# Optimization experiments

Measured on AMD Instinct MI355X. Metric: run time of the kernel, lower is better.

## Reference

```python
import jax, jax.numpy as jnp
import numpy as np

B, N, T, D, H = 32, 64, 16, 256, 256  # batch, actors, frames, feat dim, hidden_dim


def setup_inputs() -> dict:
    key = jax.random.key(0)
    ks = jax.random.split(key, 6)
    s = lambda fan: 1.0 / np.sqrt(fan)
    return {
        "x": jax.random.normal(ks[0], (B, N, T, D), jnp.float32),
        "W1_t": jax.random.normal(ks[1], (T * D, H), jnp.float32) * s(T * D),
        "b1_t": jnp.zeros((H,), jnp.float32),
        "W2_t": jax.random.normal(ks[2], (H, H), jnp.float32) * s(H),
        "b2_t": jnp.zeros((H,), jnp.float32),
        "W1_i": jax.random.normal(ks[3], (2 * H, H), jnp.float32) * s(2 * H),
        "b1_i": jnp.zeros((H,), jnp.float32),
        "W2_i": jax.random.normal(ks[4], (H, H), jnp.float32) * s(H),
        "b2_i": jnp.zeros((H,), jnp.float32),
    }


def reference(x, W1_t, b1_t, W2_t, b2_t, W1_i, b1_i, W2_i, b2_i):
    b, n, t, d = x.shape
    # STTR_trans output is immediately detached in the original; modeled as
    # identity + stop_gradient (view(N,B,T,-1) then view-back is a no-op on data).
    pf = jax.lax.stop_gradient(x)  # [B, N, T, D]

    # time_track_projection: MLP(T*D -> H -> H), ReLU between layers, no BN, eval dropout.
    h = jax.nn.relu(pf.reshape(b * n, t * d) @ W1_t + b1_t)
    person_feature = (h @ W2_t + b2_t).reshape(b, n, -1)  # [B, N, H]

    # relation_indexes: row-major enumeration of ordered pairs (i, j), j != i.
    # tem1 row N*i+j holds feature i, tem2 row N*i+j holds feature j.
    ii, jj = np.nonzero(~np.eye(n, dtype=bool))  # each [N*(N-1)], row-major order
    pair = jnp.concatenate(
        [person_feature[:, ii, :], person_feature[:, jj, :]], axis=-1
    )  # [B, N*(N-1), 2H] -- gather avoids materializing the full N*N grid

    # interaction_track_projection: MLP(2H -> H -> H)
    hi = jax.nn.relu(pair @ W1_i + b1_i)
    relation_feature = hi @ W2_i + b2_i  # [B, N*(N-1), H]

    return relation_feature, pf, person_feature
```

## Files before the change

### kernel.cpp

```cpp
#include <hip/hip_runtime.h>
#include <stdint.h>

typedef unsigned short u16;
typedef __attribute__((ext_vector_type(4))) float f32x4;
typedef __attribute__((ext_vector_type(8))) short bf16x8;
typedef __attribute__((ext_vector_type(4))) unsigned short u16x4;

#define DEV static __device__ __forceinline__

DEV u16 f2bf(float f) {
  union { float f; uint32_t u; } v; v.f = f;
  uint32_t u = v.u;
  return (u16)((u + 0x7FFFu + ((u >> 16) & 1u)) >> 16);
}

__global__ __launch_bounds__(256) void k_fuse_cast(const float* __restrict__ x,
                                                   float* __restrict__ pf,
                                                   u16* __restrict__ xb) {
  int i = blockIdx.x * 256 + threadIdx.x;
  f32x4 v = *(const f32x4*)(x + i * 4);
  *(f32x4*)(pf + i * 4) = v;
  u16x4 o;
  #pragma unroll
  for (int e = 0; e < 4; ++e) o[e] = f2bf(v[e]);
  *(u16x4*)(xb + i * 4) = o;
}

__global__ __launch_bounds__(256) void k_prep(const float* __restrict__ W1t,
                                              const float* __restrict__ W2t,
                                              const float* __restrict__ W1i,
                                              const float* __restrict__ W2i,
                                              const float* __restrict__ b2t,
                                              const float* __restrict__ b1i,
                                              u16* __restrict__ W1T,
                                              u16* __restrict__ W2iT,
                                              u16* __restrict__ WcatT,
                                              float* __restrict__ biascat) {
  __shared__ u16 tile[64][65];
  __shared__ float col[256];
  int b = blockIdx.x;
  int t = threadIdx.x;
  if (b < 272) {
    const float* in;
    u16* out;
    int R, C, bb;
    if (b < 256) { in = W1t; out = W1T; R = 4096; C = 256; bb = b; }
    else         { in = W2i; out = W2iT; R = 256;  C = 256; bb = b - 256; }
    int tr = (bb >> 2) * 64, tc = (bb & 3) * 64;
    int lr = t & 63;
    #pragma unroll
    for (int it = 0; it < 16; ++it) {
      int r = it * 4 + (t >> 6);
      tile[r][lr] = f2bf(in[(tr + r) * C + tc + lr]);
    }
    __syncthreads();
    #pragma unroll
    for (int it = 0; it < 16; ++it) {
      int c = it * 4 + (t >> 6);
      out[(tc + c) * R + tr + lr] = tile[lr][c];
    }
    return;
  }
  if (b < 1040) {
    int n = b - 272;
    int k = t;
    if (n < 256) {
      WcatT[n * 256 + k] = f2bf(W2t[k * 256 + n]);
      return;
    }
    int off = (n < 512) ? 0 : 256;
    int c = n & 255;
    col[k] = W1i[(off + k) * 256 + c];
    __syncthreads();
    const float* wrow = W2t + k * 256;
    float acc = 0.f;
    #pragma unroll 4
    for (int m = 0; m < 256; ++m) acc += wrow[m] * col[m];
    WcatT[n * 256 + k] = f2bf(acc);
    return;
  }
  int n = (b - 1040) * 256 + t;
  float v;
  if (n < 256) {
    v = b2t[n];
  } else {
    int off = (n < 512) ? 0 : 256;
    int c = n & 255;
    float acc = (n < 512) ? 0.f : b1i[c];
    for (int k = 0; k < 256; ++k) acc += b2t[k] * W1i[(off + k) * 256 + c];
    v = acc;
  }
  biascat[n] = v;
}

__global__ __launch_bounds__(256) void k_gemm1(const u16* __restrict__ A,
                                               const u16* __restrict__ BT,
                                               float* __restrict__ part) {
  int w = threadIdx.x >> 6, l = threadIdx.x & 63;
  int wr = w >> 1, wc = w & 1;
  int m0 = blockIdx.x * 64 + wr * 32;
  int n0 = blockIdx.y * 128 + wc * 64;
  int k0 = blockIdx.z * 1024 + ((l >> 4) * 8);
  const u16* pa0 = A + (m0 + (l & 15)) * 4096 + k0;
  const u16* pb0 = BT + (n0 + (l & 15)) * 4096 + k0;
  f32x4 acc[2][4] = {};
  for (int ks = 0; ks < 32; ++ks) {
    bf16x8 a[2], bfr[4];
    #pragma unroll
    for (int mf = 0; mf < 2; ++mf)
      a[mf] = *(const bf16x8*)(pa0 + mf * 16 * 4096 + ks * 32);
    #pragma unroll
    for (int nf = 0; nf < 4; ++nf)
      bfr[nf] = *(const bf16x8*)(pb0 + nf * 16 * 4096 + ks * 32);
    #pragma unroll
    for (int mf = 0; mf < 2; ++mf)
      #pragma unroll
      for (int nf = 0; nf < 4; ++nf)
        acc[mf][nf] = __builtin_amdgcn_mfma_f32_16x16x32_bf16(bfr[nf], a[mf], acc[mf][nf], 0, 0, 0);
  }
  float* out = part + blockIdx.z * (2048 * 256);
  #pragma unroll
  for (int mf = 0; mf < 2; ++mf) {
    int row = m0 + mf * 16 + (l & 15);
    #pragma unroll
    for (int nf = 0; nf < 4; ++nf) {
      int colv = n0 + nf * 16 + ((l >> 4) * 4);
      *(f32x4*)(out + row * 256 + colv) = acc[mf][nf];
    }
  }
}

__global__ __launch_bounds__(256) void k_reduce_h(const float* __restrict__ part,
                                                  const float* __restrict__ b1t,
                                                  u16* __restrict__ hb) {
  int i = blockIdx.x * 256 + threadIdx.x;
  int e = i * 4;
  f32x4 s = *(const f32x4*)(part + e);
  s += *(const f32x4*)(part + 1 * 2048 * 256 + e);
  s += *(const f32x4*)(part + 2 * 2048 * 256 + e);
  s += *(const f32x4*)(part + 3 * 2048 * 256 + e);
  f32x4 bb = *(const f32x4*)(b1t + (e & 255));
  u16x4 o;
  #pragma unroll
  for (int r = 0; r < 4; ++r) {
    float v = fmaxf(s[r] + bb[r], 0.f);
    o[r] = f2bf(v);
  }
  *(u16x4*)(hb + e) = o;
}

__global__ __launch_bounds__(256) void k_gemm3(const u16* __restrict__ A,
                                               const u16* __restrict__ BT,
                                               const float* __restrict__ biascat,
                                               float* __restrict__ person,
                                               float* __restrict__ Apr,
                                               float* __restrict__ Bpr) {
  int w = threadIdx.x >> 6, l = threadIdx.x & 63;
  int row = blockIdx.x * 64 + w * 16 + (l & 15);
  int coln = blockIdx.y * 64;
  int k0 = (l >> 4) * 8;
  const u16* pa = A + row * 256 + k0;
  const u16* pb0 = BT + (coln + (l & 15)) * 256 + k0;
  f32x4 acc[4] = {};
  #pragma unroll
  for (int ks = 0; ks < 8; ++ks) {
    bf16x8 a = *(const bf16x8*)(pa + ks * 32);
    #pragma unroll
    for (int nf = 0; nf < 4; ++nf) {
      bf16x8 b = *(const bf16x8*)(pb0 + nf * 16 * 256 + ks * 32);
      acc[nf] = __builtin_amdgcn_mfma_f32_16x16x32_bf16(b, a, acc[nf], 0, 0, 0);
    }
  }
  float* dst;
  int cbase = coln;
  if (coln < 256) { dst = person; }
  else if (coln < 512) { dst = Apr; cbase = coln - 256; }
  else { dst = Bpr; cbase = coln - 512; }
  #pragma unroll
  for (int nf = 0; nf < 4; ++nf) {
    int lc = nf * 16 + ((l >> 4) * 4);
    f32x4 bias4 = *(const f32x4*)(biascat + coln + lc);
    *(f32x4*)(dst + row * 256 + cbase + lc) = acc[nf] + bias4;
  }
}

__global__ __launch_bounds__(512, 2) void k_pair_gemm(const float* __restrict__ Apr,
                                                      const float* __restrict__ Bpr,
                                                      const u16* __restrict__ W2iT,
                                                      const float* __restrict__ b2i,
                                                      float* __restrict__ rel) {
  __shared__ u16 hi[128 * 264];
  int t = threadIdx.x;
  int lane = t & 63;
  int R0 = blockIdx.x * 128;
  #pragma unroll
  for (int it = 0; it < 16; ++it) {
    int r = it * 8 + (t >> 6);
    int R = R0 + r;
    int b = R / 4032;
    int q = R - b * 4032;
    int i = q / 63;
    int rem = q - i * 63;
    int j = rem + (rem >= i ? 1 : 0);
    f32x4 va = *(const f32x4*)(Apr + (b * 64 + i) * 256 + lane * 4);
    f32x4 vb = *(const f32x4*)(Bpr + (b * 64 + j) * 256 + lane * 4);
    u16x4 o;
    #pragma unroll
    for (int e = 0; e < 4; ++e) o[e] = f2bf(fmaxf(va[e] + vb[e], 0.f));
    *(u16x4*)(&hi[r * 264 + lane * 4]) = o;
  }
  __syncthreads();
  int wid = t >> 6;
  int wr = wid >> 2, wc = wid & 3;
  f32x4 acc[4][4] = {};
  int arow0 = wr * 64 + (lane & 15);
  int koff = (lane >> 4) * 8;
  const u16* pb0 = W2iT + (wc * 64 + (lane & 15)) * 256 + koff;
  #pragma unroll 2
  for (int ks = 0; ks < 8; ++ks) {
    bf16x8 a[4], bfr[4];
    #pragma unroll
    for (int mf = 0; mf < 4; ++mf)
      a[mf] = *(const bf16x8*)(&hi[(arow0 + mf * 16) * 264 + ks * 32 + koff]);
    #pragma unroll
    for (int nf = 0; nf < 4; ++nf)
      bfr[nf] = *(const bf16x8*)(pb0 + nf * 16 * 256 + ks * 32);
    #pragma unroll
    for (int mf = 0; mf < 4; ++mf)
      #pragma unroll
      for (int nf = 0; nf < 4; ++nf)
        acc[mf][nf] = __builtin_amdgcn_mfma_f32_16x16x32_bf16(bfr[nf], a[mf], acc[mf][nf], 0, 0, 0);
  }
  #pragma unroll
  for (int mf = 0; mf < 4; ++mf) {
    int row = R0 + wr * 64 + mf * 16 + (lane & 15);
    #pragma unroll
    for (int nf = 0; nf < 4; ++nf) {
      int gc = wc * 64 + nf * 16 + ((lane >> 4) * 4);
      f32x4 bias4 = *(const f32x4*)(b2i + gc);
      *(f32x4*)(rel + row * 256 + gc) = acc[mf][nf] + bias4;
    }
  }
}


extern "C" void kernel_launch(void* const* d_in, const int* in_sizes, int n_in,
                              void* d_out, int out_size, void* d_ws, size_t ws_size,
                              hipStream_t stream) {
  const float* x   = (const float*)d_in[0];
  const float* W1t = (const float*)d_in[1];
  const float* b1t = (const float*)d_in[2];
  const float* W2t = (const float*)d_in[3];
  const float* b2t = (const float*)d_in[4];
  const float* W1i = (const float*)d_in[5];
  const float* b1i = (const float*)d_in[6];
  const float* W2i = (const float*)d_in[7];
  const float* b2i = (const float*)d_in[8];

  float* out = (float*)d_out;
  float* rel = out;
  float* pf = out + 33030144;
  float* person = out + 41418752;

  char* ws = (char*)d_ws;
  u16*   x_bf    = (u16*)(ws + 0);
  u16*   W1T     = (u16*)(ws + 16777216);
  u16*   WcatT   = (u16*)(ws + 18874368);
  u16*   W2iT    = (u16*)(ws + 19267584);
  float* biascat = (float*)(ws + 19398656);
  u16*   h_bf    = (u16*)(ws + 19402752);
  float* Apr     = (float*)(ws + 20451328);
  float* Bpr     = (float*)(ws + 22548480);
  float* part    = (float*)(ws + 24645632);

  k_fuse_cast<<<8192, 256, 0, stream>>>(x, pf, x_bf);
  k_prep<<<1043, 256, 0, stream>>>(W1t, W2t, W1i, W2i, b2t, b1i,
                                   W1T, W2iT, WcatT, biascat);
  k_gemm1<<<dim3(32, 2, 4), 256, 0, stream>>>(x_bf, W1T, part);
  k_reduce_h<<<512, 256, 0, stream>>>(part, b1t, h_bf);
  k_gemm3<<<dim3(32, 12), 256, 0, stream>>>(h_bf, WcatT, biascat, person, Apr, Bpr);
  k_pair_gemm<<<1008, 512, 0, stream>>>(Apr, Bpr, W2iT, b2i, rel);
}
```

Baseline: 135.3 us.

## Merge cast and prep kernels, raise gemm1 split-K to 16 with bf16 partials

Folds the x copy/cast kernel into the weight-prep kernel so one launch does both, with each thread now handling 8 elements. The first GEMM is re-tiled from 256 blocks (split-K 4) to 1024 blocks (split-K 16) so more CUs are busy, and partial sums are stored as bf16 to keep partial-buffer traffic down. The reduce kernel sums 16 bf16 partials in fp32. The bias loads in the pair GEMM are hoisted out of the store loop. Rounding each partial to bf16 adds accuracy error to the hidden activations.

```diff
diff --git a/kernel.cpp b/kernel.cpp
--- a/kernel.cpp
+++ b/kernel.cpp
@@ -14,32 +14,42 @@
   return (u16)((u + 0x7FFFu + ((u >> 16) & 1u)) >> 16);
 }
 
-__global__ __launch_bounds__(256) void k_fuse_cast(const float* __restrict__ x,
-                                                   float* __restrict__ pf,
-                                                   u16* __restrict__ xb) {
-  int i = blockIdx.x * 256 + threadIdx.x;
-  f32x4 v = *(const f32x4*)(x + i * 4);
-  *(f32x4*)(pf + i * 4) = v;
-  u16x4 o;
-  #pragma unroll
-  for (int e = 0; e < 4; ++e) o[e] = f2bf(v[e]);
-  *(u16x4*)(xb + i * 4) = o;
-}
-
-__global__ __launch_bounds__(256) void k_prep(const float* __restrict__ W1t,
-                                              const float* __restrict__ W2t,
-                                              const float* __restrict__ W1i,
-                                              const float* __restrict__ W2i,
-                                              const float* __restrict__ b2t,
-                                              const float* __restrict__ b1i,
-                                              u16* __restrict__ W1T,
-                                              u16* __restrict__ W2iT,
-                                              u16* __restrict__ WcatT,
-                                              float* __restrict__ biascat) {
+DEV float bf2f(u16 u) {
+  union { uint32_t u; float f; } v; v.u = ((uint32_t)u) << 16;
+  return v.f;
+}
+
+__global__ __launch_bounds__(256) void k_pre(const float* __restrict__ x,
+                                             float* __restrict__ pf,
+                                             u16* __restrict__ xb,
+                                             const float* __restrict__ W1t,
+                                             const float* __restrict__ W2t,
+                                             const float* __restrict__ W1i,
+                                             const float* __restrict__ W2i,
+                                             const float* __restrict__ b2t,
+                                             const float* __restrict__ b1i,
+                                             u16* __restrict__ W1T,
+                                             u16* __restrict__ W2iT,
+                                             u16* __restrict__ WcatT,
+                                             float* __restrict__ biascat) {
   __shared__ u16 tile[64][65];
   __shared__ float col[256];
   int b = blockIdx.x;
   int t = threadIdx.x;
+  if (b < 4096) {
+    int i = b * 256 + t;
+    #pragma unroll
+    for (int h = 0; h < 2; ++h) {
+      f32x4 v = *(const f32x4*)(x + i * 8 + h * 4);
+      *(f32x4*)(pf + i * 8 + h * 4) = v;
+      u16x4 o;
+      #pragma unroll
+      for (int e = 0; e < 4; ++e) o[e] = f2bf(v[e]);
+      *(u16x4*)(xb + i * 8 + h * 4) = o;
+    }
+    return;
+  }
+  b -= 4096;
   if (b < 272) {
     const float* in;
     u16* out;
@@ -95,16 +105,16 @@
 
 __global__ __launch_bounds__(256) void k_gemm1(const u16* __restrict__ A,
                                                const u16* __restrict__ BT,
-                                               float* __restrict__ part) {
+                                               u16* __restrict__ part) {
   int w = threadIdx.x >> 6, l = threadIdx.x & 63;
-  int wr = w >> 1, wc = w & 1;
-  int m0 = blockIdx.x * 64 + wr * 32;
-  int n0 = blockIdx.y * 128 + wc * 64;
-  int k0 = blockIdx.z * 1024 + ((l >> 4) * 8);
+  int m0 = blockIdx.x * 32;
+  int n0 = w * 64;
+  int k0 = blockIdx.y * 256 + ((l >> 4) * 8);
   const u16* pa0 = A + (m0 + (l & 15)) * 4096 + k0;
   const u16* pb0 = BT + (n0 + (l & 15)) * 4096 + k0;
   f32x4 acc[2][4] = {};
-  for (int ks = 0; ks < 32; ++ks) {
+  #pragma unroll 2
+  for (int ks = 0; ks < 8; ++ks) {
     bf16x8 a[2], bfr[4];
     #pragma unroll
     for (int mf = 0; mf < 2; ++mf)
@@ -118,34 +128,37 @@
       for (int nf = 0; nf < 4; ++nf)
         acc[mf][nf] = __builtin_amdgcn_mfma_f32_16x16x32_bf16(bfr[nf], a[mf], acc[mf][nf], 0, 0, 0);
   }
-  float* out = part + blockIdx.z * (2048 * 256);
+  u16* out = part + blockIdx.y * (2048 * 256);
   #pragma unroll
   for (int mf = 0; mf < 2; ++mf) {
     int row = m0 + mf * 16 + (l & 15);
     #pragma unroll
     for (int nf = 0; nf < 4; ++nf) {
       int colv = n0 + nf * 16 + ((l >> 4) * 4);
-      *(f32x4*)(out + row * 256 + colv) = acc[mf][nf];
-    }
-  }
-}
-
-__global__ __launch_bounds__(256) void k_reduce_h(const float* __restrict__ part,
+      u16x4 o;
+      #pragma unroll
+      for (int r = 0; r < 4; ++r) o[r] = f2bf(acc[mf][nf][r]);
+      *(u16x4*)(out + row * 256 + colv) = o;
+    }
+  }
+}
+
+__global__ __launch_bounds__(256) void k_reduce_h(const u16* __restrict__ part,
                                                   const float* __restrict__ b1t,
                                                   u16* __restrict__ hb) {
   int i = blockIdx.x * 256 + threadIdx.x;
   int e = i * 4;
-  f32x4 s = *(const f32x4*)(part + e);
-  s += *(const f32x4*)(part + 1 * 2048 * 256 + e);
-  s += *(const f32x4*)(part + 2 * 2048 * 256 + e);
-  s += *(const f32x4*)(part + 3 * 2048 * 256 + e);
+  f32x4 s = {};
+  #pragma unroll
+  for (int z = 0; z < 16; ++z) {
+    u16x4 p = *(const u16x4*)(part + z * (2048 * 256) + e);
+    #pragma unroll
+    for (int r = 0; r < 4; ++r) s[r] += bf2f(p[r]);
+  }
   f32x4 bb = *(const f32x4*)(b1t + (e & 255));
   u16x4 o;
   #pragma unroll
-  for (int r = 0; r < 4; ++r) {
-    float v = fmaxf(s[r] + bb[r], 0.f);
-    o[r] = f2bf(v);
-  }
+  for (int r = 0; r < 4; ++r) o[r] = f2bf(fmaxf(s[r] + bb[r], 0.f));
   *(u16x4*)(hb + e) = o;
 }
 
@@ -231,14 +244,17 @@
       for (int nf = 0; nf < 4; ++nf)
         acc[mf][nf] = __builtin_amdgcn_mfma_f32_16x16x32_bf16(bfr[nf], a[mf], acc[mf][nf], 0, 0, 0);
   }
+  f32x4 bias4[4];
+  #pragma unroll
+  for (int nf = 0; nf < 4; ++nf)
+    bias4[nf] = *(const f32x4*)(b2i + wc * 64 + nf * 16 + ((lane >> 4) * 4));
   #pragma unroll
   for (int mf = 0; mf < 4; ++mf) {
     int row = R0 + wr * 64 + mf * 16 + (lane & 15);
     #pragma unroll
     for (int nf = 0; nf < 4; ++nf) {
       int gc = wc * 64 + nf * 16 + ((lane >> 4) * 4);
-      f32x4 bias4 = *(const f32x4*)(b2i + gc);
-      *(f32x4*)(rel + row * 256 + gc) = acc[mf][nf] + bias4;
+      *(f32x4*)(rel + row * 256 + gc) = acc[mf][nf] + bias4[nf];
     }
   }
 }
@@ -271,12 +287,11 @@
   u16*   h_bf    = (u16*)(ws + 19402752);
   float* Apr     = (float*)(ws + 20451328);
   float* Bpr     = (float*)(ws + 22548480);
-  float* part    = (float*)(ws + 24645632);
-
-  k_fuse_cast<<<8192, 256, 0, stream>>>(x, pf, x_bf);
-  k_prep<<<1043, 256, 0, stream>>>(W1t, W2t, W1i, W2i, b2t, b1i,
-                                   W1T, W2iT, WcatT, biascat);
-  k_gemm1<<<dim3(32, 2, 4), 256, 0, stream>>>(x_bf, W1T, part);
+  u16*   part    = (u16*)(ws + 24645632);
+
+  k_pre<<<5139, 256, 0, stream>>>(x, pf, x_bf, W1t, W2t, W1i, W2i, b2t, b1i,
+                                  W1T, W2iT, WcatT, biascat);
+  k_gemm1<<<dim3(64, 16), 256, 0, stream>>>(x_bf, W1T, part);
   k_reduce_h<<<512, 256, 0, stream>>>(part, b1t, h_bf);
   k_gemm3<<<dim3(32, 12), 256, 0, stream>>>(h_bf, WcatT, biascat, person, Apr, Bpr);
   k_pair_gemm<<<1008, 512, 0, stream>>>(Apr, Bpr, W2iT, b2i, rel);
```

New measurement: 145.6 us. 1.08x slower.
